# Kernel tuning notes

Hardware: AMD Instinct MI355X
Metric: run time of the kernel (lower is better)

The kernel has to match this reference:

```python
import jax, jax.numpy as jnp
import numpy as np

D_MODEL = 1024
N_HEADS = 16
D_K = D_MODEL // N_HEADS
THETA = 10000.0
B, S = 2, 2048


def _rope(x):
    # x: [B, H, S, Dh], interleaved-pair RoPE with positions arange(S)
    Dh = x.shape[-1]
    inv_freq = 1.0 / (THETA ** (jnp.arange(0, Dh, 2, dtype=jnp.float32) / Dh))  # [Dh/2]
    pos = jnp.arange(x.shape[-2], dtype=jnp.float32)
    ang = pos[:, None] * inv_freq[None, :]                      # [S, Dh/2]
    cos = jnp.repeat(jnp.cos(ang), 2, axis=-1).astype(x.dtype)  # [S, Dh]
    sin = jnp.repeat(jnp.sin(ang), 2, axis=-1).astype(x.dtype)
    # rotate pairs: (x_2k, x_2k+1) -> (-x_2k+1, x_2k)
    xp = x.reshape(*x.shape[:-1], Dh // 2, 2)
    rot = jnp.stack((-xp[..., 1], xp[..., 0]), axis=-1).reshape(x.shape)
    return x * cos + rot * sin


def setup_inputs() -> dict:
    key = jax.random.key(0)
    ks = jax.random.split(key, 5)
    std = (2.0 / (D_MODEL + D_MODEL)) ** 0.5
    return {
        "x": jax.random.normal(ks[0], (B, S, D_MODEL), dtype=jnp.float32),
        "wq": jax.random.normal(ks[1], (D_MODEL, D_MODEL), dtype=jnp.float32) * std,
        "wk": jax.random.normal(ks[2], (D_MODEL, D_MODEL), dtype=jnp.float32) * std,
        "wv": jax.random.normal(ks[3], (D_MODEL, D_MODEL), dtype=jnp.float32) * std,
        "wo": jax.random.normal(ks[4], (D_MODEL, D_MODEL), dtype=jnp.float32) * std,
    }


def reference(x, wq, wk, wv, wo):
    b, s, _ = x.shape
    def split_heads(t):
        return t.reshape(b, s, N_HEADS, D_K).transpose(0, 2, 1, 3)  # [B,H,S,Dk]
    # Linear: y = x @ W.T  (weights stored [out, in])
    q = split_heads(jnp.einsum('bsd,od->bso', x, wq))
    k = split_heads(jnp.einsum('bsd,od->bso', x, wk))
    v = split_heads(jnp.einsum('bsd,od->bso', x, wv))
    q = _rope(q)
    k = _rope(k)
    scores = jnp.einsum('bhqd,bhkd->bhqk', q, k) / jnp.sqrt(jnp.asarray(D_K, x.dtype))
    causal = jnp.tril(jnp.ones((s, s), dtype=bool))
    scores = jnp.where(causal[None, None], scores, -jnp.inf)
    attn = jax.nn.softmax(scores, axis=-1)
    out = jnp.einsum('bhqk,bhkd->bhqd', attn, v)
    out = out.transpose(0, 2, 1, 3).reshape(b, s, D_MODEL)
    return jnp.einsum('bsd,od->bso', out, wo)
```

## Files before the change

### kernel.cpp

```cpp
#include <hip/hip_runtime.h>


typedef unsigned short u16;
typedef __attribute__((ext_vector_type(8))) short short8;
typedef __attribute__((ext_vector_type(4))) float float4v;

typedef const __attribute__((address_space(1))) void GV;
typedef __attribute__((address_space(3))) void LV;

#define VSTR 72
#define QSCL 0.18033688011112042f

__device__ __forceinline__ u16 f2b(float f) {
    union { float f; unsigned int i; } t; t.f = f;
    unsigned int r = t.i + 0x7fffu + ((t.i >> 16) & 1u);
    return (u16)(r >> 16);
}

__global__ __launch_bounds__(256) void cvt_all(
    const float4* __restrict__ x,  const float4* __restrict__ wq,
    const float4* __restrict__ wk, const float4* __restrict__ wv,
    const float4* __restrict__ wo,
    u16* __restrict__ xb, u16* __restrict__ wcat, u16* __restrict__ wob)
{
    const int i = blockIdx.x * 256 + threadIdx.x;
    const float4* s; u16* d; int off;
    if (i < 524288) { s = x; d = xb; off = i; }
    else {
        const int widx = i - 524288;
        const int w = widx >> 17, o = widx & 131071;
        switch (w) {
            case 0:  s = wq; d = wcat;              break;
            case 1:  s = wk; d = wcat + (1 << 20);  break;
            case 2:  s = wv; d = wcat + (2 << 20);  break;
            default: s = wo; d = wob;               break;
        }
        off = o;
    }
    float4 a = s[2 * off], b = s[2 * off + 1];
    u16 t[8] = {f2b(a.x), f2b(a.y), f2b(a.z), f2b(a.w),
                f2b(b.x), f2b(b.y), f2b(b.z), f2b(b.w)};
    reinterpret_cast<int4*>(d)[off] = *reinterpret_cast<int4*>(t);
}

__global__ __launch_bounds__(256) void rope_tab(float2* __restrict__ tab) {
    const int i = blockIdx.x * 256 + threadIdx.x;
    const int pos = i >> 5, fi = i & 31;
    const float freq = exp2f((float)fi * -0.4152410118609203f);
    float sn, cs; sincosf((float)pos * freq, &sn, &cs);
    tab[i] = make_float2(cs, sn);
}

__global__ __launch_bounds__(512) void gemm_qkv(
    const u16* __restrict__ X, const u16* __restrict__ Wb,
    u16* __restrict__ Yq, u16* __restrict__ Yk, u16* __restrict__ Yv,
    const float2* __restrict__ tab)
{
    __shared__ u16 As[2][256 * 64];
    __shared__ u16 Bs[2][192 * 64];

    const int tid  = threadIdx.x;
    const int wave = tid >> 6;
    const int lane = tid & 63;
    const int quad = lane >> 4;
    const int l16  = lane & 15;
    const int wm = (wave >> 2) * 128;
    const int wn = (wave & 3) * 48;
    const int g = blockIdx.x;
    const int rr = g >> 3;
    const int m0 = ((g & 7) * 2 + (rr >> 4)) * 256;
    const int n0 = (rr & 15) * 192;
    const int lrow = lane >> 3;
    const int cg8  = (lane & 7) ^ lrow;

    float4v acc[8][3];
#pragma unroll
    for (int mt = 0; mt < 8; mt++)
#pragma unroll
        for (int nt = 0; nt < 3; nt++) acc[mt][nt] = (float4v){0.f, 0.f, 0.f, 0.f};

    auto stage = [&](int bsel, int kb) {
#pragma unroll
        for (int t = 0; t < 4; t++) {
            const int I = wave * 4 + t;
            const u16* gp = X + (size_t)(m0 + I * 8 + lrow) * 1024 + kb + cg8 * 8;
            __builtin_amdgcn_global_load_lds((GV*)gp, (LV*)&As[bsel][I * 512], 16, 0, 0);
        }
#pragma unroll
        for (int t = 0; t < 3; t++) {
            const int I = wave * 3 + t;
            const u16* gp = Wb + (size_t)(n0 + I * 8 + lrow) * 1024 + kb + cg8 * 8;
            __builtin_amdgcn_global_load_lds((GV*)gp, (LV*)&Bs[bsel][I * 512], 16, 0, 0);
        }
    };

    stage(0, 0);
    __syncthreads();

    for (int kbi = 0; kbi < 16; kbi++) {
        const int cur = kbi & 1;
        if (kbi < 15) stage(cur ^ 1, (kbi + 1) * 64);
#pragma unroll
        for (int ks = 0; ks < 2; ks++) {
            const int su = ((ks * 4 + quad) ^ (l16 & 7)) * 8;
            short8 af[8], bf[3];
#pragma unroll
            for (int t = 0; t < 8; t++)
                af[t] = *reinterpret_cast<const short8*>(&As[cur][(wm + t * 16 + l16) * 64 + su]);
#pragma unroll
            for (int t = 0; t < 3; t++)
                bf[t] = *reinterpret_cast<const short8*>(&Bs[cur][(wn + t * 16 + l16) * 64 + su]);
#pragma unroll
            for (int mt = 0; mt < 8; mt++)
#pragma unroll
                for (int nt = 0; nt < 3; nt++)
                    acc[mt][nt] = __builtin_amdgcn_mfma_f32_16x16x32_bf16(af[mt], bf[nt], acc[mt][nt], 0, 0, 0);
        }
        __syncthreads();
    }

#pragma unroll
    for (int nt = 0; nt < 3; nt++) {
        const int cg = n0 + wn + nt * 16 + l16;
        const int buf = cg >> 10;
        const int c = cg & 1023;
        u16* dst = (buf == 0) ? Yq : ((buf == 1) ? Yk : Yv);
        const bool rp = (buf < 2);
        const float scl = (buf == 0) ? QSCL : 1.0f;
        const int fi = (cg & 63) >> 1;
#pragma unroll
        for (int mt = 0; mt < 8; mt++)
#pragma unroll
            for (int r = 0; r < 4; r++) {
                const int row = m0 + wm + mt * 16 + quad * 4 + r;
                float v = acc[mt][nt][r];
                if (rp) {
                    const float2 t = tab[((row & 2047) << 5) + fi];
                    const float partner = __shfl_xor(v, 1);
                    v = (l16 & 1) ? fmaf(v, t.x,  partner * t.y)
                                  : fmaf(v, t.x, -partner * t.y);
                }
                dst[(size_t)row * 1024 + c] = f2b(v * scl);
            }
    }
}

template<int NT, int NBLK>
__global__ __launch_bounds__(256) void gemm_tile(
    const u16* __restrict__ X, const u16* __restrict__ Wb,
    float* __restrict__ Yf)
{
    __shared__ u16 As[128 * 64];
    __shared__ u16 Bs[NT * 32 * 64];

    const int tid  = threadIdx.x;
    const int wave = tid >> 6;
    const int lane = tid & 63;
    const int quad = lane >> 4;
    const int l16  = lane & 15;
    const int wm = (wave >> 1) * 64, wn = (wave & 1) * (NT * 16);
    const int g = blockIdx.x;
    const int rr = g >> 3;
    const int m0 = ((g & 7) * 4 + rr / NBLK) * 128;
    const int n0 = (rr % NBLK) * (NT * 32);
    const int lrow = lane >> 3;
    const int cg8  = (lane & 7) ^ lrow;

    float4v acc[4][NT];
#pragma unroll
    for (int mt = 0; mt < 4; mt++)
#pragma unroll
        for (int nt = 0; nt < NT; nt++) acc[mt][nt] = (float4v){0.f, 0.f, 0.f, 0.f};

    for (int kb = 0; kb < 1024; kb += 64) {
        __syncthreads();
#pragma unroll
        for (int t = 0; t < 4; t++) {
            const int I = wave * 4 + t;
            const u16* gp = X + (size_t)(m0 + I * 8 + lrow) * 1024 + kb + cg8 * 8;
            __builtin_amdgcn_global_load_lds((GV*)gp, (LV*)&As[I * 512], 16, 0, 0);
        }
#pragma unroll
        for (int t = 0; t < NT; t++) {
            const int I = wave * NT + t;
            const u16* gp = Wb + (size_t)(n0 + I * 8 + lrow) * 1024 + kb + cg8 * 8;
            __builtin_amdgcn_global_load_lds((GV*)gp, (LV*)&Bs[I * 512], 16, 0, 0);
        }
        __syncthreads();
#pragma unroll
        for (int ks = 0; ks < 2; ks++) {
            const int su = ((ks * 4 + quad) ^ (l16 & 7)) * 8;
            short8 af[4], bf[NT];
#pragma unroll
            for (int t = 0; t < 4; t++)
                af[t] = *reinterpret_cast<const short8*>(&As[(wm + t * 16 + l16) * 64 + su]);
#pragma unroll
            for (int t = 0; t < NT; t++)
                bf[t] = *reinterpret_cast<const short8*>(&Bs[(wn + t * 16 + l16) * 64 + su]);
#pragma unroll
            for (int mt = 0; mt < 4; mt++)
#pragma unroll
                for (int nt = 0; nt < NT; nt++)
                    acc[mt][nt] = __builtin_amdgcn_mfma_f32_16x16x32_bf16(af[mt], bf[nt], acc[mt][nt], 0, 0, 0);
        }
    }

#pragma unroll
    for (int nt = 0; nt < NT; nt++) {
        const int col = n0 + wn + nt * 16 + l16;
#pragma unroll
        for (int mt = 0; mt < 4; mt++)
#pragma unroll
            for (int r = 0; r < 4; r++) {
                const int row = m0 + wm + mt * 16 + quad * 4 + r;
                Yf[(size_t)row * 1024 + col] = acc[mt][nt][r];
            }
    }
}

__global__ __launch_bounds__(256, 2) void attn_kernel(
    const u16* Q, const u16* __restrict__ K,
    const u16* __restrict__ V, u16* O)
{
    __shared__ __align__(16) u16 Vt[2][64 * VSTR];

    const int tid  = threadIdx.x;
    const int wave = tid >> 6;
    const int lane = tid & 63;
    const int quad = lane >> 4;
    const int l16  = lane & 15;
    const int g = blockIdx.x;
    const int xcd = g & 7, slot = g >> 3;
    const int G = (slot >> 4) * 8 + xcd;
    const int qtA = slot & 15;
    const int qtB = 31 - qtA;
    const int b = G & 1, h = G >> 1;
    const size_t base = ((size_t)b * 2048) * 1024 + (size_t)h * 64;

    short8 qfA[2], qfB[2];
    {
        const size_t ra = base + (size_t)(qtA * 64 + wave * 16 + l16) * 1024;
        qfA[0] = *reinterpret_cast<const short8*>(Q + ra + quad * 8);
        qfA[1] = *reinterpret_cast<const short8*>(Q + ra + 32 + quad * 8);
        const size_t rb = base + (size_t)(qtB * 64 + wave * 16 + l16) * 1024;
        qfB[0] = *reinterpret_cast<const short8*>(Q + rb + quad * 8);
        qfB[1] = *reinterpret_cast<const short8*>(Q + rb + 32 + quad * 8);
    }

    float4v oA[4], oB[4];
#pragma unroll
    for (int i = 0; i < 4; i++) { oA[i] = (float4v){0.f,0.f,0.f,0.f}; oB[i] = (float4v){0.f,0.f,0.f,0.f}; }
    float sA = 0.f, sB = 0.f;

    const int srow = tid >> 2;
    const int cb   = (tid & 3) << 4;
    const int sxw  = srow ^ cb;

    const u16* Vp = V + base + (size_t)srow * 1024 + cb;
    const u16* kbase = K + base + (size_t)l16 * 1024 + quad * 8;
    int4 vr0 = *reinterpret_cast<const int4*>(Vp);
    int4 vr1 = *reinterpret_cast<const int4*>(Vp + 8);
    short8 kn[4][2], kc[4][2], vf[4][2];
#pragma unroll
    for (int nt = 0; nt < 4; nt++)
#pragma unroll
        for (int ks = 0; ks < 2; ks++)
            kn[nt][ks] = *reinterpret_cast<const short8*>(kbase + (size_t)(nt * 16) * 1024 + ks * 32);

    {
        const u16* a = reinterpret_cast<const u16*>(&vr0);
        const u16* c = reinterpret_cast<const u16*>(&vr1);
#pragma unroll
        for (int e = 0; e < 8; e++) Vt[0][(cb + e) * VSTR + sxw] = a[e];
#pragma unroll
        for (int e = 0; e < 8; e++) Vt[0][(cb + 8 + e) * VSTR + sxw] = c[e];
    }
    vr0 = *reinterpret_cast<const int4*>(Vp + 65536);
    vr1 = *reinterpret_cast<const int4*>(Vp + 65536 + 8);

    const int qloc = wave * 16 + l16;

    auto qk = [&](const short8 (&qf)[2], float4v (&sacc)[4]) {
#pragma unroll
        for (int nt = 0; nt < 4; nt++) {
            sacc[nt] = (float4v){0.f, 0.f, 0.f, 0.f};
#pragma unroll
            for (int ks = 0; ks < 2; ks++)
                sacc[nt] = __builtin_amdgcn_mfma_f32_16x16x32_bf16(kc[nt][ks], qf[ks], sacc[nt], 0, 0, 0);
        }
    };
    auto smx = [&](const float4v (&sacc)[4], float &sr, short8 (&pa)[2], bool diag) {
        unsigned int w[4][2];
#pragma unroll
        for (int nt = 0; nt < 4; nt++) {
            float p[4];
#pragma unroll
            for (int r = 0; r < 4; r++) {
                float sv = sacc[nt][r];
                if (diag && (nt * 16 + quad * 4 + r > qloc)) sv = -1e30f;
                p[r] = exp2f(sv);
                sr += p[r];
            }
            asm("v_cvt_pk_bf16_f32 %0, %1, %2" : "=v"(w[nt][0]) : "v"(p[0]), "v"(p[1]));
            asm("v_cvt_pk_bf16_f32 %0, %1, %2" : "=v"(w[nt][1]) : "v"(p[2]), "v"(p[3]));
        }
        union { unsigned int u[4]; short8 s8; } t;
        t.u[0] = w[0][0]; t.u[1] = w[0][1]; t.u[2] = w[1][0]; t.u[3] = w[1][1];
        pa[0] = t.s8;
        t.u[0] = w[2][0]; t.u[1] = w[2][1]; t.u[2] = w[3][0]; t.u[3] = w[3][1];
        pa[1] = t.s8;
    };
    auto pv = [&](const short8 (&pa)[2], float4v (&oc)[4]) {
#pragma unroll
        for (int ks = 0; ks < 2; ks++)
#pragma unroll
            for (int dt = 0; dt < 4; dt++)
                oc[dt] = __builtin_amdgcn_mfma_f32_16x16x32_bf16(pa[ks], vf[dt][ks], oc[dt], 0, 0, 0);
    };

    for (int j = 0; j <= qtB; j++) {
        __syncthreads();
        if (j < qtB) {
            u16* D = Vt[(j + 1) & 1];
            const u16* a = reinterpret_cast<const u16*>(&vr0);
            const u16* c = reinterpret_cast<const u16*>(&vr1);
#pragma unroll
            for (int e = 0; e < 8; e++) D[(cb + e) * VSTR + sxw] = a[e];
#pragma unroll
            for (int e = 0; e < 8; e++) D[(cb + 8 + e) * VSTR + sxw] = c[e];
        }
#pragma unroll
        for (int nt = 0; nt < 4; nt++)
#pragma unroll
            for (int ks = 0; ks < 2; ks++) kc[nt][ks] = kn[nt][ks];
        if (j < qtB) {
            if (j + 2 <= qtB) {
                vr0 = *reinterpret_cast<const int4*>(Vp + (size_t)(j + 2) * 65536);
                vr1 = *reinterpret_cast<const int4*>(Vp + (size_t)(j + 2) * 65536 + 8);
            }
            const u16* kb2 = kbase + (size_t)(j + 1) * 65536;
#pragma unroll
            for (int nt = 0; nt < 4; nt++)
#pragma unroll
                for (int ks = 0; ks < 2; ks++)
                    kn[nt][ks] = *reinterpret_cast<const short8*>(kb2 + (size_t)(nt * 16) * 1024 + ks * 32);
        }
        {
            const u16* B = Vt[j & 1];
#pragma unroll
            for (int dt = 0; dt < 4; dt++) {
                const int rb = (dt * 16 + l16) * VSTR;
#pragma unroll
                for (int ks = 0; ks < 2; ks++) {
                    const int k1 = (ks * 32 + quad * 4) ^ (dt << 4);
                    const int k2 = (ks * 32 + 16 + quad * 4) ^ (dt << 4);
                    union { struct { uint2 lo, hi; } p; short8 s8; } u;
                    u.p.lo = *reinterpret_cast<const uint2*>(&B[rb + k1]);
                    u.p.hi = *reinterpret_cast<const uint2*>(&B[rb + k2]);
                    vf[dt][ks] = u.s8;
                }
            }
        }

        if (j <= qtA) {
            float4v xA[4], xB[4];
            qk(qfA, xA);
            qk(qfB, xB);
            short8 paA[2], paB[2];
            smx(xA, sA, paA, j == qtA);
            smx(xB, sB, paB, false);
            pv(paA, oA);
            pv(paB, oB);
        } else {
            float4v xB[4];
            qk(qfB, xB);
            short8 paB[2];
            smx(xB, sB, paB, j == qtB);
            pv(paB, oB);
        }
    }

    float tA = sA, tB = sB;
    tA += __shfl_xor(tA, 16); tA += __shfl_xor(tA, 32);
    tB += __shfl_xor(tB, 16); tB += __shfl_xor(tB, 32);
#pragma unroll
    for (int r = 0; r < 4; r++) {
        const int rl = quad * 4 + r;
        const float invA = 1.0f / __shfl(tA, rl);
        const float invB = 1.0f / __shfl(tB, rl);
        const size_t rowA = base + (size_t)(qtA * 64 + wave * 16 + rl) * 1024;
        const size_t rowB = base + (size_t)(qtB * 64 + wave * 16 + rl) * 1024;
#pragma unroll
        for (int dt = 0; dt < 4; dt++) {
            O[rowA + dt * 16 + l16] = f2b(oA[dt][r] * invA);
            O[rowB + dt * 16 + l16] = f2b(oB[dt][r] * invB);
        }
    }
}

extern "C" void kernel_launch(void* const* d_in, const int* in_sizes, int n_in,
                              void* d_out, int out_size, void* d_ws, size_t ws_size,
                              hipStream_t stream) {
    (void)in_sizes; (void)n_in; (void)out_size; (void)ws_size;
    const float* x  = (const float*)d_in[0];
    const float* wq = (const float*)d_in[1];
    const float* wk = (const float*)d_in[2];
    const float* wv = (const float*)d_in[3];
    const float* wo = (const float*)d_in[4];

    const size_t MN = (size_t)4096 * 1024;

    u16* xb   = (u16*)d_out;
    u16* wcat = xb + MN;
    float2* tab = (float2*)(wcat + (size_t)3072 * 1024);
    u16* qbuf = (u16*)d_ws;
    u16* kbuf = qbuf + MN;
    u16* vbuf = kbuf + MN;
    u16* wob  = vbuf + MN;

    cvt_all<<<4096, 256, 0, stream>>>((const float4*)x, (const float4*)wq,
                                      (const float4*)wk, (const float4*)wv,
                                      (const float4*)wo, xb, wcat, wob);
    rope_tab<<<256, 256, 0, stream>>>(tab);
    gemm_qkv<<<256, 512, 0, stream>>>(xb, wcat, qbuf, kbuf, vbuf, tab);
    attn_kernel<<<512, 256, 0, stream>>>(qbuf, kbuf, vbuf, qbuf);
    gemm_tile<2, 16><<<512, 256, 0, stream>>>(qbuf, wob, (float*)d_out);
}
```

Baseline: 217.4 us.

## Split attention key range across two blocks with atomic partial merge

Each (head, paired q-tile) work item is now split into two blocks along the key dimension, doubling the grid to 1024 blocks. This raises parallelism and evens out per-block work. The B tile's unnormalized output and row sums are accumulated with float atomics into a zeroed scratch area, and a new merge_norm kernel then normalizes and writes bf16 output. The cost is two extra kernel launches, atomic traffic and scratch memory reused from the output buffer. No max-subtraction is used, so merging plain sums is valid.

```diff
diff --git a/kernel.cpp b/kernel.cpp
--- a/kernel.cpp
+++ b/kernel.cpp
@@ -51,6 +51,10 @@
     tab[i] = make_float2(cs, sn);
 }
 
+__global__ __launch_bounds__(256) void zerows(float4* __restrict__ p) {
+    p[blockIdx.x * 256 + threadIdx.x] = (float4){0.f, 0.f, 0.f, 0.f};
+}
+
 __global__ __launch_bounds__(512) void gemm_qkv(
     const u16* __restrict__ X, const u16* __restrict__ Wb,
     u16* __restrict__ Yq, u16* __restrict__ Yk, u16* __restrict__ Yv,
@@ -220,7 +224,8 @@
 
 __global__ __launch_bounds__(256, 2) void attn_kernel(
     const u16* Q, const u16* __restrict__ K,
-    const u16* __restrict__ V, u16* O)
+    const u16* __restrict__ V, u16* O,
+    float* __restrict__ P, float* __restrict__ S)
 {
     __shared__ __align__(16) u16 Vt[2][64 * VSTR];
 
@@ -231,17 +236,24 @@
     const int l16  = lane & 15;
     const int g = blockIdx.x;
     const int xcd = g & 7, slot = g >> 3;
-    const int G = (slot >> 4) * 8 + xcd;
-    const int qtA = slot & 15;
-    const int qtB = 31 - qtA;
+    const int e   = slot & 1;
+    const int p   = (slot >> 1) & 15;
+    const int G   = (slot >> 5) * 8 + xcd;
+    const int qtA = p;
+    const int qtB = 31 - p;
+    const int jbeg = e ? (15 - qtA) : 0;
+    const int jend = e ? (31 - qtA) : 15;
+    const int L = jend - jbeg;
     const int b = G & 1, h = G >> 1;
     const size_t base = ((size_t)b * 2048) * 1024 + (size_t)h * 64;
 
     short8 qfA[2], qfB[2];
-    {
+    if (!e) {
         const size_t ra = base + (size_t)(qtA * 64 + wave * 16 + l16) * 1024;
         qfA[0] = *reinterpret_cast<const short8*>(Q + ra + quad * 8);
         qfA[1] = *reinterpret_cast<const short8*>(Q + ra + 32 + quad * 8);
+    }
+    {
         const size_t rb = base + (size_t)(qtB * 64 + wave * 16 + l16) * 1024;
         qfB[0] = *reinterpret_cast<const short8*>(Q + rb + quad * 8);
         qfB[1] = *reinterpret_cast<const short8*>(Q + rb + 32 + quad * 8);
@@ -258,25 +270,25 @@
 
     const u16* Vp = V + base + (size_t)srow * 1024 + cb;
     const u16* kbase = K + base + (size_t)l16 * 1024 + quad * 8;
-    int4 vr0 = *reinterpret_cast<const int4*>(Vp);
-    int4 vr1 = *reinterpret_cast<const int4*>(Vp + 8);
+    int4 vr0 = *reinterpret_cast<const int4*>(Vp + (size_t)jbeg * 65536);
+    int4 vr1 = *reinterpret_cast<const int4*>(Vp + (size_t)jbeg * 65536 + 8);
     short8 kn[4][2], kc[4][2], vf[4][2];
 #pragma unroll
     for (int nt = 0; nt < 4; nt++)
 #pragma unroll
         for (int ks = 0; ks < 2; ks++)
-            kn[nt][ks] = *reinterpret_cast<const short8*>(kbase + (size_t)(nt * 16) * 1024 + ks * 32);
+            kn[nt][ks] = *reinterpret_cast<const short8*>(kbase + (size_t)jbeg * 65536 + (size_t)(nt * 16) * 1024 + ks * 32);
 
     {
         const u16* a = reinterpret_cast<const u16*>(&vr0);
         const u16* c = reinterpret_cast<const u16*>(&vr1);
 #pragma unroll
-        for (int e = 0; e < 8; e++) Vt[0][(cb + e) * VSTR + sxw] = a[e];
-#pragma unroll
-        for (int e = 0; e < 8; e++) Vt[0][(cb + 8 + e) * VSTR + sxw] = c[e];
-    }
-    vr0 = *reinterpret_cast<const int4*>(Vp + 65536);
-    vr1 = *reinterpret_cast<const int4*>(Vp + 65536 + 8);
+        for (int ee = 0; ee < 8; ee++) Vt[0][(cb + ee) * VSTR + sxw] = a[ee];
+#pragma unroll
+        for (int ee = 0; ee < 8; ee++) Vt[0][(cb + 8 + ee) * VSTR + sxw] = c[ee];
+    }
+    vr0 = *reinterpret_cast<const int4*>(Vp + (size_t)(jbeg + 1) * 65536);
+    vr1 = *reinterpret_cast<const int4*>(Vp + (size_t)(jbeg + 1) * 65536 + 8);
 
     const int qloc = wave * 16 + l16;
 
@@ -293,16 +305,16 @@
         unsigned int w[4][2];
 #pragma unroll
         for (int nt = 0; nt < 4; nt++) {
-            float p[4];
+            float pp[4];
 #pragma unroll
             for (int r = 0; r < 4; r++) {
                 float sv = sacc[nt][r];
                 if (diag && (nt * 16 + quad * 4 + r > qloc)) sv = -1e30f;
-                p[r] = exp2f(sv);
-                sr += p[r];
-            }
-            asm("v_cvt_pk_bf16_f32 %0, %1, %2" : "=v"(w[nt][0]) : "v"(p[0]), "v"(p[1]));
-            asm("v_cvt_pk_bf16_f32 %0, %1, %2" : "=v"(w[nt][1]) : "v"(p[2]), "v"(p[3]));
+                pp[r] = exp2f(sv);
+                sr += pp[r];
+            }
+            asm("v_cvt_pk_bf16_f32 %0, %1, %2" : "=v"(w[nt][0]) : "v"(pp[0]), "v"(pp[1]));
+            asm("v_cvt_pk_bf16_f32 %0, %1, %2" : "=v"(w[nt][1]) : "v"(pp[2]), "v"(pp[3]));
         }
         union { unsigned int u[4]; short8 s8; } t;
         t.u[0] = w[0][0]; t.u[1] = w[0][1]; t.u[2] = w[1][0]; t.u[3] = w[1][1];
@@ -318,23 +330,24 @@
                 oc[dt] = __builtin_amdgcn_mfma_f32_16x16x32_bf16(pa[ks], vf[dt][ks], oc[dt], 0, 0, 0);
     };
 
-    for (int j = 0; j <= qtB; j++) {
+    for (int jj = 0; jj <= L; jj++) {
+        const int j = jbeg + jj;
         __syncthreads();
-        if (j < qtB) {
-            u16* D = Vt[(j + 1) & 1];
+        if (jj < L) {
+            u16* D = Vt[(jj + 1) & 1];
             const u16* a = reinterpret_cast<const u16*>(&vr0);
             const u16* c = reinterpret_cast<const u16*>(&vr1);
 #pragma unroll
-            for (int e = 0; e < 8; e++) D[(cb + e) * VSTR + sxw] = a[e];
-#pragma unroll
-            for (int e = 0; e < 8; e++) D[(cb + 8 + e) * VSTR + sxw] = c[e];
+            for (int ee = 0; ee < 8; ee++) D[(cb + ee) * VSTR + sxw] = a[ee];
+#pragma unroll
+            for (int ee = 0; ee < 8; ee++) D[(cb + 8 + ee) * VSTR + sxw] = c[ee];
         }
 #pragma unroll
         for (int nt = 0; nt < 4; nt++)
 #pragma unroll
             for (int ks = 0; ks < 2; ks++) kc[nt][ks] = kn[nt][ks];
-        if (j < qtB) {
-            if (j + 2 <= qtB) {
+        if (jj < L) {
+            if (jj + 2 <= L) {
                 vr0 = *reinterpret_cast<const int4*>(Vp + (size_t)(j + 2) * 65536);
                 vr1 = *reinterpret_cast<const int4*>(Vp + (size_t)(j + 2) * 65536 + 8);
             }
@@ -345,8 +358,11 @@
                 for (int ks = 0; ks < 2; ks++)
                     kn[nt][ks] = *reinterpret_cast<const short8*>(kb2 + (size_t)(nt * 16) * 1024 + ks * 32);
         }
-        {
-            const u16* B = Vt[j & 1];
+
+        const bool actA = (!e) && (j <= qtA);
+        const bool actB = e ? true : (j <= 14 - qtA);
+        if (actA || actB) {
+            const u16* Bt = Vt[jj & 1];
 #pragma unroll
             for (int dt = 0; dt < 4; dt++) {
                 const int rb = (dt * 16 + l16) * VSTR;
@@ -354,48 +370,69 @@
                 for (int ks = 0; ks < 2; ks++) {
                     const int k1 = (ks * 32 + quad * 4) ^ (dt << 4);
                     const int k2 = (ks * 32 + 16 + quad * 4) ^ (dt << 4);
-                    union { struct { uint2 lo, hi; } p; short8 s8; } u;
-                    u.p.lo = *reinterpret_cast<const uint2*>(&B[rb + k1]);
-                    u.p.hi = *reinterpret_cast<const uint2*>(&B[rb + k2]);
+                    union { struct { uint2 lo, hi; } pr; short8 s8; } u;
+                    u.pr.lo = *reinterpret_cast<const uint2*>(&Bt[rb + k1]);
+                    u.pr.hi = *reinterpret_cast<const uint2*>(&Bt[rb + k2]);
                     vf[dt][ks] = u.s8;
                 }
             }
-        }
-
-        if (j <= qtA) {
-            float4v xA[4], xB[4];
-            qk(qfA, xA);
-            qk(qfB, xB);
-            short8 paA[2], paB[2];
-            smx(xA, sA, paA, j == qtA);
-            smx(xB, sB, paB, false);
-            pv(paA, oA);
-            pv(paB, oB);
-        } else {
-            float4v xB[4];
-            qk(qfB, xB);
-            short8 paB[2];
-            smx(xB, sB, paB, j == qtB);
-            pv(paB, oB);
-        }
-    }
-
-    float tA = sA, tB = sB;
-    tA += __shfl_xor(tA, 16); tA += __shfl_xor(tA, 32);
+            if (actA) {
+                float4v xA[4]; short8 paA[2];
+                qk(qfA, xA);
+                smx(xA, sA, paA, j == qtA);
+                pv(paA, oA);
+            }
+            if (actB) {
+                float4v xB[4]; short8 paB[2];
+                qk(qfB, xB);
+                smx(xB, sB, paB, j == qtB);
+                pv(paB, oB);
+            }
+        }
+    }
+
+    if (!e) {
+        float tA = sA;
+        tA += __shfl_xor(tA, 16); tA += __shfl_xor(tA, 32);
+#pragma unroll
+        for (int r = 0; r < 4; r++) {
+            const int rl = quad * 4 + r;
+            const float invA = 1.0f / __shfl(tA, rl);
+            const size_t rowA = base + (size_t)(qtA * 64 + wave * 16 + rl) * 1024;
+#pragma unroll
+            for (int dt = 0; dt < 4; dt++)
+                O[rowA + dt * 16 + l16] = f2b(oA[dt][r] * invA);
+        }
+    }
+    float tB = sB;
     tB += __shfl_xor(tB, 16); tB += __shfl_xor(tB, 32);
-#pragma unroll
-    for (int r = 0; r < 4; r++) {
-        const int rl = quad * 4 + r;
-        const float invA = 1.0f / __shfl(tA, rl);
-        const float invB = 1.0f / __shfl(tB, rl);
-        const size_t rowA = base + (size_t)(qtA * 64 + wave * 16 + rl) * 1024;
-        const size_t rowB = base + (size_t)(qtB * 64 + wave * 16 + rl) * 1024;
-#pragma unroll
-        for (int dt = 0; dt < 4; dt++) {
-            O[rowA + dt * 16 + l16] = f2b(oA[dt][r] * invA);
-            O[rowB + dt * 16 + l16] = f2b(oB[dt][r] * invB);
-        }
-    }
+    float* Pb = P + (size_t)((G * 16 + (qtB - 16)) * 64) * 64;
+#pragma unroll
+    for (int dt = 0; dt < 4; dt++)
+#pragma unroll
+        for (int r = 0; r < 4; r++)
+            atomicAdd(&Pb[(wave * 16 + quad * 4 + r) * 64 + dt * 16 + l16], oB[dt][r]);
+    if (quad == 0)
+        atomicAdd(&S[(G * 16 + (qtB - 16)) * 64 + wave * 16 + l16], tB);
+}
+
+__global__ __launch_bounds__(256) void merge_norm(
+    const float* __restrict__ P, const float* __restrict__ S,
+    u16* __restrict__ O)
+{
+    const int i = blockIdx.x * 256 + threadIdx.x;
+    const int d4  = i & 15;
+    const int row = (i >> 4) & 63;
+    const int t   = (i >> 10) & 15;
+    const int G   = i >> 14;
+    const float4 v = *reinterpret_cast<const float4*>(
+        &P[((size_t)((G * 16 + t) * 64 + row)) * 64 + d4 * 4]);
+    const float inv = 1.0f / S[(G * 16 + t) * 64 + row];
+    const int b = G & 1, h = G >> 1;
+    const size_t addr = (size_t)b * 2048 * 1024
+                      + (size_t)((t + 16) * 64 + row) * 1024 + h * 64 + d4 * 4;
+    u16 o4[4] = {f2b(v.x * inv), f2b(v.y * inv), f2b(v.z * inv), f2b(v.w * inv)};
+    *reinterpret_cast<uint2*>(&O[addr]) = *reinterpret_cast<uint2*>(o4);
 }
 
 extern "C" void kernel_launch(void* const* d_in, const int* in_sizes, int n_in,
@@ -413,6 +450,8 @@
     u16* xb   = (u16*)d_out;
     u16* wcat = xb + MN;
     float2* tab = (float2*)(wcat + (size_t)3072 * 1024);
+    float* Pp = (float*)d_out;
+    float* Sp = Pp + (size_t)32 * 16 * 64 * 64;
     u16* qbuf = (u16*)d_ws;
     u16* kbuf = qbuf + MN;
     u16* vbuf = kbuf + MN;
@@ -423,6 +462,8 @@
                                       (const float4*)wo, xb, wcat, wob);
     rope_tab<<<256, 256, 0, stream>>>(tab);
     gemm_qkv<<<256, 512, 0, stream>>>(xb, wcat, qbuf, kbuf, vbuf, tab);
-    attn_kernel<<<512, 256, 0, stream>>>(qbuf, kbuf, vbuf, qbuf);
+    zerows<<<2080, 256, 0, stream>>>((float4*)Pp);
+    attn_kernel<<<1024, 256, 0, stream>>>(qbuf, kbuf, vbuf, qbuf, Pp, Sp);
+    merge_norm<<<2048, 256, 0, stream>>>(Pp, Sp, qbuf);
     gemm_tile<2, 16><<<512, 256, 0, stream>>>(qbuf, wob, (float*)d_out);
 }
```

Measured after the change: 237.3 us. 1.09x slower.

## Fold RoPE table into convert kernel and double-buffer output projection GEMM

Applied to the files above, without the earlier changes.

Merges the rope_tab kernel into cvt_all as extra blocks, removing one kernel launch. Replaces the output projection GEMM with a 512-thread, 256x64-tile version that double-buffers LDS, prefetching the next K-slice while computing the current one, and syncs once per iteration instead of twice. This is meant to hide global-to-LDS load latency and cut launch overhead, at the cost of more LDS use per block and half as many blocks (256 instead of 512).

```diff
diff --git a/kernel.cpp b/kernel.cpp
--- a/kernel.cpp
+++ b/kernel.cpp
@@ -21,9 +21,19 @@
     const float4* __restrict__ x,  const float4* __restrict__ wq,
     const float4* __restrict__ wk, const float4* __restrict__ wv,
     const float4* __restrict__ wo,
-    u16* __restrict__ xb, u16* __restrict__ wcat, u16* __restrict__ wob)
+    u16* __restrict__ xb, u16* __restrict__ wcat, u16* __restrict__ wob,
+    float2* __restrict__ tab)
 {
-    const int i = blockIdx.x * 256 + threadIdx.x;
+    const int blk = blockIdx.x;
+    if (blk >= 4096) {
+        const int i = (blk - 4096) * 256 + threadIdx.x;
+        const int pos = i >> 5, fi = i & 31;
+        const float freq = exp2f((float)fi * -0.4152410118609203f);
+        float sn, cs; sincosf((float)pos * freq, &sn, &cs);
+        tab[i] = make_float2(cs, sn);
+        return;
+    }
+    const int i = blk * 256 + threadIdx.x;
     const float4* s; u16* d; int off;
     if (i < 524288) { s = x; d = xb; off = i; }
     else {
@@ -41,14 +51,6 @@
     u16 t[8] = {f2b(a.x), f2b(a.y), f2b(a.z), f2b(a.w),
                 f2b(b.x), f2b(b.y), f2b(b.z), f2b(b.w)};
     reinterpret_cast<int4*>(d)[off] = *reinterpret_cast<int4*>(t);
-}
-
-__global__ __launch_bounds__(256) void rope_tab(float2* __restrict__ tab) {
-    const int i = blockIdx.x * 256 + threadIdx.x;
-    const int pos = i >> 5, fi = i & 31;
-    const float freq = exp2f((float)fi * -0.4152410118609203f);
-    float sn, cs; sincosf((float)pos * freq, &sn, &cs);
-    tab[i] = make_float2(cs, sn);
 }
 
 __global__ __launch_bounds__(512) void gemm_qkv(
@@ -145,68 +147,73 @@
     }
 }
 
-template<int NT, int NBLK>
-__global__ __launch_bounds__(256) void gemm_tile(
+__global__ __launch_bounds__(512) void gemm_proj(
     const u16* __restrict__ X, const u16* __restrict__ Wb,
     float* __restrict__ Yf)
 {
-    __shared__ u16 As[128 * 64];
-    __shared__ u16 Bs[NT * 32 * 64];
+    __shared__ u16 As[2][256 * 64];
+    __shared__ u16 Bs[2][64 * 64];
 
     const int tid  = threadIdx.x;
     const int wave = tid >> 6;
     const int lane = tid & 63;
     const int quad = lane >> 4;
     const int l16  = lane & 15;
-    const int wm = (wave >> 1) * 64, wn = (wave & 1) * (NT * 16);
+    const int wm = (wave >> 1) * 64;
+    const int wn = (wave & 1) * 32;
     const int g = blockIdx.x;
     const int rr = g >> 3;
-    const int m0 = ((g & 7) * 4 + rr / NBLK) * 128;
-    const int n0 = (rr % NBLK) * (NT * 32);
+    const int m0 = ((g & 7) * 2 + (rr >> 4)) * 256;
+    const int n0 = (rr & 15) * 64;
     const int lrow = lane >> 3;
     const int cg8  = (lane & 7) ^ lrow;
 
-    float4v acc[4][NT];
+    float4v acc[4][2];
 #pragma unroll
     for (int mt = 0; mt < 4; mt++)
 #pragma unroll
-        for (int nt = 0; nt < NT; nt++) acc[mt][nt] = (float4v){0.f, 0.f, 0.f, 0.f};
-
-    for (int kb = 0; kb < 1024; kb += 64) {
-        __syncthreads();
+        for (int nt = 0; nt < 2; nt++) acc[mt][nt] = (float4v){0.f, 0.f, 0.f, 0.f};
+
+    auto stage = [&](int bsel, int kb) {
 #pragma unroll
         for (int t = 0; t < 4; t++) {
             const int I = wave * 4 + t;
             const u16* gp = X + (size_t)(m0 + I * 8 + lrow) * 1024 + kb + cg8 * 8;
-            __builtin_amdgcn_global_load_lds((GV*)gp, (LV*)&As[I * 512], 16, 0, 0);
-        }
-#pragma unroll
-        for (int t = 0; t < NT; t++) {
-            const int I = wave * NT + t;
-            const u16* gp = Wb + (size_t)(n0 + I * 8 + lrow) * 1024 + kb + cg8 * 8;
-            __builtin_amdgcn_global_load_lds((GV*)gp, (LV*)&Bs[I * 512], 16, 0, 0);
-        }
-        __syncthreads();
+            __builtin_amdgcn_global_load_lds((GV*)gp, (LV*)&As[bsel][I * 512], 16, 0, 0);
+        }
+        {
+            const u16* gp = Wb + (size_t)(n0 + wave * 8 + lrow) * 1024 + kb + cg8 * 8;
+            __builtin_amdgcn_global_load_lds((GV*)gp, (LV*)&Bs[bsel][wave * 512], 16, 0, 0);
+        }
+    };
+
+    stage(0, 0);
+    __syncthreads();
+
+    for (int kbi = 0; kbi < 16; kbi++) {
+        const int cur = kbi & 1;
+        if (kbi < 15) stage(cur ^ 1, (kbi + 1) * 64);
 #pragma unroll
         for (int ks = 0; ks < 2; ks++) {
             const int su = ((ks * 4 + quad) ^ (l16 & 7)) * 8;
-            short8 af[4], bf[NT];
+            short8 af[4], bf[2];
 #pragma unroll
             for (int t = 0; t < 4; t++)
-                af[t] = *reinterpret_cast<const short8*>(&As[(wm + t * 16 + l16) * 64 + su]);
-#pragma unroll
-            for (int t = 0; t < NT; t++)
-                bf[t] = *reinterpret_cast<const short8*>(&Bs[(wn + t * 16 + l16) * 64 + su]);
+                af[t] = *reinterpret_cast<const short8*>(&As[cur][(wm + t * 16 + l16) * 64 + su]);
+#pragma unroll
+            for (int t = 0; t < 2; t++)
+                bf[t] = *reinterpret_cast<const short8*>(&Bs[cur][(wn + t * 16 + l16) * 64 + su]);
 #pragma unroll
             for (int mt = 0; mt < 4; mt++)
 #pragma unroll
-                for (int nt = 0; nt < NT; nt++)
+                for (int nt = 0; nt < 2; nt++)
                     acc[mt][nt] = __builtin_amdgcn_mfma_f32_16x16x32_bf16(af[mt], bf[nt], acc[mt][nt], 0, 0, 0);
         }
-    }
-
-#pragma unroll
-    for (int nt = 0; nt < NT; nt++) {
+        __syncthreads();
+    }
+
+#pragma unroll
+    for (int nt = 0; nt < 2; nt++) {
         const int col = n0 + wn + nt * 16 + l16;
 #pragma unroll
         for (int mt = 0; mt < 4; mt++)
@@ -418,11 +425,10 @@
     u16* vbuf = kbuf + MN;
     u16* wob  = vbuf + MN;
 
-    cvt_all<<<4096, 256, 0, stream>>>((const float4*)x, (const float4*)wq,
+    cvt_all<<<4352, 256, 0, stream>>>((const float4*)x, (const float4*)wq,
                                       (const float4*)wk, (const float4*)wv,
-                                      (const float4*)wo, xb, wcat, wob);
-    rope_tab<<<256, 256, 0, stream>>>(tab);
+                                      (const float4*)wo, xb, wcat, wob, tab);
     gemm_qkv<<<256, 512, 0, stream>>>(xb, wcat, qbuf, kbuf, vbuf, tab);
     attn_kernel<<<512, 256, 0, stream>>>(qbuf, kbuf, vbuf, qbuf);
-    gemm_tile<2, 16><<<512, 256, 0, stream>>>(qbuf, wob, (float*)d_out);
-}
+    gemm_proj<<<256, 512, 0, stream>>>(qbuf, wob, (float*)d_out);
+}
```

Result: no change. 218.2 us (+0.4%).
